# Kernel tuning notes

Measured on AMD Instinct MI355X. Metric: run time of the kernel, lower is better.

The kernel has to match this reference:

```python
import jax, jax.numpy as jnp
import numpy as np

N_NODES = 100000
N_EDGES = 1600000
N_FEAT = 128
HIDDEN = 128
EMB = 256
N_GROUPS = 16
N_GRAPHS = 512


def gcn_conv(x, edge_index, W, b, num_nodes):
    # PyG GCNConv: x' = D^{-1/2} (A + I) D^{-1/2} (x W) + b
    h = x @ W                                   # [N, out]
    loop = jnp.arange(num_nodes, dtype=edge_index.dtype)
    src = jnp.concatenate([edge_index[0], loop])
    dst = jnp.concatenate([edge_index[1], loop])
    ones = jnp.ones(src.shape[0], dtype=h.dtype)
    deg = jax.ops.segment_sum(ones, dst, num_segments=num_nodes)  # >=1 due to self loops
    dinv = jax.lax.rsqrt(deg)
    norm = dinv[src] * dinv[dst]                # [E+N]
    msg = h[src] * norm[:, None]                # gather + scale
    out = jax.ops.segment_sum(msg, dst, num_segments=num_nodes)   # scatter-add
    return out + b


def global_mean_pool(x, batch, num_graphs):
    s = jax.ops.segment_sum(x, batch, num_segments=num_graphs)
    cnt = jax.ops.segment_sum(jnp.ones(x.shape[0], dtype=x.dtype), batch, num_segments=num_graphs)
    return s / jnp.maximum(cnt, 1.0)[:, None]


def setup_inputs() -> dict:
    key = jax.random.key(0)
    ks = jax.random.split(key, 10)
    x = jax.random.normal(ks[0], (N_NODES, N_FEAT), dtype=jnp.float32)
    edge_index = jax.random.randint(ks[1], (2, N_EDGES), 0, N_NODES, dtype=jnp.int64 if jax.config.jax_enable_x64 else jnp.int32)
    batch = jnp.sort(jax.random.randint(ks[2], (N_NODES,), 0, N_GRAPHS))
    def glorot(k, shape):
        lim = np.sqrt(6.0 / (shape[0] + shape[1]))
        return jax.random.uniform(k, shape, jnp.float32, -lim, lim)
    W1 = glorot(ks[3], (N_FEAT, HIDDEN)); b1 = jnp.zeros((HIDDEN,), jnp.float32)
    W2 = glorot(ks[4], (HIDDEN, EMB));    b2 = jnp.zeros((EMB,), jnp.float32)
    Wg = glorot(ks[5], (EMB, N_GROUPS));  bg = jnp.zeros((N_GROUPS,), jnp.float32)
    return {"x": x, "edge_index": edge_index, "batch": batch, "num_graphs": N_GRAPHS,
            "W1": W1, "b1": b1, "W2": W2, "b2": b2, "Wg": Wg, "bg": bg}


def reference(x, edge_index, batch, num_graphs, W1, b1, W2, b2, Wg, bg):
    n = x.shape[0]
    h = jax.nn.relu(gcn_conv(x, edge_index, W1, b1, n))
    # dropout(p=0.5) is identity in eval mode
    h = gcn_conv(h, edge_index, W2, b2, n)
    emb = global_mean_pool(h, batch, num_graphs)      # [G, EMB]
    group_logits = emb @ Wg + bg                      # [G, N_GROUPS]
    return (emb, group_logits)
```

## Files before the change

### kernel.cpp

```cpp
#include <hip/hip_runtime.h>
#include <hip/hip_fp16.h>


#define TPB 256
#define CHUNK 4096
#define MAXB 512
#define SUBS 8

typedef _Float16 half8 __attribute__((ext_vector_type(8)));
typedef float floatx4 __attribute__((ext_vector_type(4)));

__device__ __forceinline__ void exscan512(int* a, int* part, int t) {
    int x0 = a[2 * t], x1 = a[2 * t + 1];
    part[t] = x0 + x1;
    __syncthreads();
    for (int off = 1; off < 256; off <<= 1) {
        int v = (t >= off) ? part[t - off] : 0;
        __syncthreads();
        part[t] += v;
        __syncthreads();
    }
    int base = (t > 0) ? part[t - 1] : 0;
    a[2 * t] = base;
    a[2 * t + 1] = base + x0;
    __syncthreads();
}

__global__ __launch_bounds__(256) void k1_bucket(const int* __restrict__ ei, int E,
                                                 int B, int nchunks,
                                                 uint2* __restrict__ sorted,
                                                 int* __restrict__ histT,
                                                 int* __restrict__ sstartT,
                                                 int* __restrict__ bucketTot) {
    __shared__ int hcnt[MAXB], hoff[MAXB], hcur[MAXB], part[256];
    int c = blockIdx.x, t = threadIdx.x;
    int e0 = c * CHUNK;
    int m = E - e0; if (m > CHUNK) m = CHUNK;
    for (int i = t; i < MAXB; i += 256) { hcnt[i] = 0; hcur[i] = 0; }
    __syncthreads();
    for (int i = t; i < m; i += 256)
        atomicAdd(&hcnt[ei[E + e0 + i] >> 8], 1);
    __syncthreads();
    for (int i = t; i < MAXB; i += 256) hoff[i] = hcnt[i];
    __syncthreads();
    exscan512(hoff, part, t);
    for (int i = t; i < B; i += 256) {
        histT[(size_t)i * nchunks + c]   = hcnt[i];
        sstartT[(size_t)i * nchunks + c] = e0 + hoff[i];
        if (hcnt[i] > 0) atomicAdd(&bucketTot[i], hcnt[i]);
    }
    __syncthreads();
    for (int i = t; i < m; i += 256) {
        int src = ei[e0 + i], dst = ei[E + e0 + i];
        int b = dst >> 8;
        int pos = e0 + hoff[b] + atomicAdd(&hcur[b], 1);
        sorted[pos] = make_uint2((unsigned)src, (unsigned)dst);
    }
}

__global__ void k2_scanB(const int* __restrict__ bucketTot, int B,
                         int* __restrict__ bucketBase) {
    __shared__ int a[MAXB], part[256];
    int t = threadIdx.x;
    a[t]       = (t < B) ? bucketTot[t] : 0;
    a[t + 256] = (t + 256 < B) ? bucketTot[t + 256] : 0;
    __syncthreads();
    exscan512(a, part, t);
    if (t < B) bucketBase[t] = a[t];
    if (t + 256 < B) bucketBase[t + 256] = a[t + 256];
    if (t == 255) bucketBase[B] = part[255];
}

#define SLICE_SETUP                                                             \
    int b = blockIdx.x, sub = blockIdx.y, t = threadIdx.x;                      \
    int cpg = (nchunks + SUBS - 1) / SUBS;                                      \
    int c0 = sub * cpg;                                                         \
    int c1 = c0 + cpg; if (c1 > nchunks) c1 = nchunks;                          \
    int nc = c1 - c0; if (nc < 0) nc = 0;                                       \
    if (t < nc) {                                                               \
        slen[t]   = histT[(size_t)b * nchunks + c0 + t];                        \
        sstart[t] = sstartT[(size_t)b * nchunks + c0 + t];                      \
    }                                                                           \
    __syncthreads();                                                            \
    if (t == 0) {                                                               \
        int run = 0;                                                            \
        for (int i2 = 0; i2 < nc; ++i2) { soff[i2] = run; run += slen[i2]; }    \
        soff[nc] = run;                                                         \
    }                                                                           \
    __syncthreads();                                                            \
    int T = soff[nc];

#define SLICE_EDGE(i)                                                           \
    int lo = 0, hi = nc - 1;                                                    \
    while (lo < hi) { int mid = (lo + hi + 1) >> 1;                             \
                      if (soff[mid] <= (i)) lo = mid; else hi = mid - 1; }      \
    uint2 e = sorted[sstart[lo] + ((i) - soff[lo])];

__global__ __launch_bounds__(256) void k3a_deg(const uint2* __restrict__ sorted,
                                               const int* __restrict__ histT,
                                               const int* __restrict__ sstartT,
                                               int* __restrict__ deg,
                                               int n, int nchunks) {
    __shared__ int slen[64], sstart[64], soff[65];
    __shared__ int ncnt[256];
    SLICE_SETUP
    ncnt[t] = 0;
    __syncthreads();
    int vb = b << 8;
    for (int i = t; i < T; i += 256) {
        SLICE_EDGE(i)
        atomicAdd(&ncnt[(int)e.y - vb], 1);
    }
    __syncthreads();
    int v = vb + t;
    if (v < n && ncnt[t] > 0) atomicAdd(&deg[v], ncnt[t]);
}

__global__ __launch_bounds__(256) void k3b_offs(const int* __restrict__ deg,
                                                const int* __restrict__ bucketBase,
                                                const int* __restrict__ batch,
                                                int* __restrict__ offs,
                                                float* __restrict__ dinv,
                                                int* __restrict__ cnt, int n) {
    __shared__ int a[512], part[256];
    int b = blockIdx.x, t = threadIdx.x;
    int v = (b << 8) + t;
    int dg = (v < n) ? deg[v] : 0;
    a[t] = dg; a[t + 256] = 0;
    __syncthreads();
    exscan512(a, part, t);
    if (v < n) {
        offs[v] = bucketBase[b] + a[t];
        dinv[v] = rsqrtf((float)(dg + 1));
        atomicAdd(&cnt[batch[v]], 1);
    }
}

__global__ __launch_bounds__(256) void k3c_scatter(const uint2* __restrict__ sorted,
                                                   const int* __restrict__ histT,
                                                   const int* __restrict__ sstartT,
                                                   const int* __restrict__ offs,
                                                   int* __restrict__ cursor,
                                                   int* __restrict__ adj, int nchunks) {
    __shared__ int slen[64], sstart[64], soff[65];
    SLICE_SETUP
    for (int i = t; i < T; i += 256) {
        SLICE_EDGE(i)
        int dst = (int)e.y;
        int pos = offs[dst] + atomicAdd(&cursor[dst], 1);
        adj[pos] = (int)e.x;
    }
}

__global__ void prep_wt(const float* __restrict__ W, __half* __restrict__ Wt) {
    int t = blockIdx.x * blockDim.x + threadIdx.x;
    int c = t & 127, k = t >> 7;
    Wt[c * 128 + k] = __float2half(W[(size_t)k * 128 + c]);
}

__global__ __launch_bounds__(256) void gemm1_mfma(const float* __restrict__ X,
                                                  const __half* __restrict__ Wt,
                                                  const float* __restrict__ dinv,
                                                  __half* __restrict__ out, int n) {
    __shared__ __align__(16) unsigned char As[64 * 128 * 2];
    __shared__ __align__(16) unsigned char Bs[128 * 128 * 2];
    int t = threadIdx.x;
    int wid = t >> 6, lane = t & 63;
    int qw = lane >> 4, lr = lane & 15;
    int rowBase = blockIdx.x * 64;

#pragma unroll
    for (int c = 0; c < 4; ++c) {
        int id = c * 256 + t;
        int r = id >> 4, kc = id & 15;
        int gr = rowBase + r;
        float4 x0, x1;
        if (gr < n) {
            const float4* src = (const float4*)(X + (size_t)gr * 128 + kc * 8);
            x0 = src[0]; x1 = src[1];
        } else {
            x0 = make_float4(0.f, 0.f, 0.f, 0.f); x1 = x0;
        }
        __half2 h0 = __floats2half2_rn(x0.x, x0.y);
        __half2 h1 = __floats2half2_rn(x0.z, x0.w);
        __half2 h2 = __floats2half2_rn(x1.x, x1.y);
        __half2 h3 = __floats2half2_rn(x1.z, x1.w);
        uint4 w;
        w.x = *(unsigned int*)&h0; w.y = *(unsigned int*)&h1;
        w.z = *(unsigned int*)&h2; w.w = *(unsigned int*)&h3;
        int byte = (r * 256 + kc * 16) ^ ((r & 7) << 4);
        *(uint4*)(As + byte) = w;
    }
#pragma unroll
    for (int c = 0; c < 8; ++c) {
        int id = c * 256 + t;
        int cr = id >> 4, kc = id & 15;
        uint4 w = *(const uint4*)(Wt + (size_t)cr * 128 + kc * 8);
        int byte = (cr * 256 + kc * 16) ^ ((cr & 7) << 4);
        *(uint4*)(Bs + byte) = w;
    }
    __syncthreads();

    floatx4 acc[4][2] = {};
#pragma unroll
    for (int ks = 0; ks < 4; ++ks) {
        int kb = ks * 32 + qw * 8;
        half8 a[4], b[2];
#pragma unroll
        for (int m = 0; m < 4; ++m) {
            int row = m * 16 + lr;
            int byte = (row * 256 + kb * 2) ^ ((row & 7) << 4);
            a[m] = *(const half8*)(As + byte);
        }
#pragma unroll
        for (int nn = 0; nn < 2; ++nn) {
            int col = wid * 32 + nn * 16 + lr;
            int byte = (col * 256 + kb * 2) ^ ((col & 7) << 4);
            b[nn] = *(const half8*)(Bs + byte);
        }
#pragma unroll
        for (int m = 0; m < 4; ++m)
#pragma unroll
            for (int nn = 0; nn < 2; ++nn)
                acc[m][nn] = __builtin_amdgcn_mfma_f32_16x16x32_f16(a[m], b[nn], acc[m][nn], 0, 0, 0);
    }

#pragma unroll
    for (int m = 0; m < 4; ++m) {
#pragma unroll
        for (int q = 0; q < 4; ++q) {
            int gr = rowBase + m * 16 + qw * 4 + q;
            if (gr < n) {
                float dv = dinv[gr];
#pragma unroll
                for (int nn = 0; nn < 2; ++nn) {
                    int col = wid * 32 + nn * 16 + lr;
                    out[(size_t)gr * 128 + col] = __float2half(acc[m][nn][q] * dv);
                }
            }
        }
    }
}

__device__ __forceinline__ void acc_h2(unsigned int rv, float2& a) {
    float2 f = __half22float2(*(__half2*)&rv);
    a.x += f.x; a.y += f.y;
}
#define ROWP(buf, u) ((const unsigned int*)((buf) + (size_t)(u) * 128))

#define PIPE_GATHER(buf)                                                        \
    int nb = d >> 3;                                                            \
    int i = nb << 3;                                                            \
    if (nb > 0) {                                                               \
        int u0 = adj[start+0], u1 = adj[start+1], u2 = adj[start+2],            \
            u3 = adj[start+3], u4 = adj[start+4], u5 = adj[start+5],            \
            u6 = adj[start+6], u7 = adj[start+7];                               \
        unsigned c0 = ROWP(buf,u0)[lane], c1 = ROWP(buf,u1)[lane];              \
        unsigned c2 = ROWP(buf,u2)[lane], c3 = ROWP(buf,u3)[lane];              \
        unsigned c4 = ROWP(buf,u4)[lane], c5 = ROWP(buf,u5)[lane];              \
        unsigned c6 = ROWP(buf,u6)[lane], c7 = ROWP(buf,u7)[lane];              \
        for (int bq = 1; bq < nb; ++bq) {                                       \
            int bs = start + (bq << 3);                                         \
            int t0 = adj[bs+0], t1 = adj[bs+1], t2 = adj[bs+2], t3 = adj[bs+3]; \
            int t4 = adj[bs+4], t5 = adj[bs+5], t6 = adj[bs+6], t7 = adj[bs+7]; \
            unsigned n0 = ROWP(buf,t0)[lane], n1 = ROWP(buf,t1)[lane];          \
            unsigned n2 = ROWP(buf,t2)[lane], n3 = ROWP(buf,t3)[lane];          \
            unsigned n4 = ROWP(buf,t4)[lane], n5 = ROWP(buf,t5)[lane];          \
            unsigned n6 = ROWP(buf,t6)[lane], n7 = ROWP(buf,t7)[lane];          \
            acc_h2(c0, a0); acc_h2(c1, a1); acc_h2(c2, a2); acc_h2(c3, a3);     \
            acc_h2(c4, a0); acc_h2(c5, a1); acc_h2(c6, a2); acc_h2(c7, a3);     \
            c0 = n0; c1 = n1; c2 = n2; c3 = n3;                                 \
            c4 = n4; c5 = n5; c6 = n6; c7 = n7;                                 \
        }                                                                       \
        acc_h2(c0, a0); acc_h2(c1, a1); acc_h2(c2, a2); acc_h2(c3, a3);         \
        acc_h2(c4, a0); acc_h2(c5, a1); acc_h2(c6, a2); acc_h2(c7, a3);         \
    }                                                                           \
    for (; i + 3 < d; i += 4) {                                                 \
        int u0 = adj[start+i+0], u1 = adj[start+i+1];                           \
        int u2 = adj[start+i+2], u3 = adj[start+i+3];                           \
        unsigned r0 = ROWP(buf,u0)[lane], r1 = ROWP(buf,u1)[lane];              \
        unsigned r2 = ROWP(buf,u2)[lane], r3 = ROWP(buf,u3)[lane];              \
        acc_h2(r0, a0); acc_h2(r1, a1); acc_h2(r2, a2); acc_h2(r3, a3);         \
    }                                                                           \
    for (; i < d; ++i) acc_h2(ROWP(buf, adj[start + i])[lane], a0);

__global__ void gather1(const __half* __restrict__ hs, const int* __restrict__ adj,
                        const int* __restrict__ offs, const int* __restrict__ deg,
                        const float* __restrict__ dinv, const float* __restrict__ b1,
                        __half* __restrict__ gs, int n) {
    int wave = threadIdx.x >> 6;
    int lane = threadIdx.x & 63;
    int v = blockIdx.x * 4 + wave;
    if (v >= n) return;
    float2 a0 = make_float2(0.f, 0.f), a1 = a0, a2 = a0, a3 = a0;
    acc_h2(ROWP(hs, v)[lane], a0);
    int start = __builtin_amdgcn_readfirstlane(offs[v]);
    int d     = __builtin_amdgcn_readfirstlane(deg[v]);
    PIPE_GATHER(hs)
    float accx = (a0.x + a1.x) + (a2.x + a3.x);
    float accy = (a0.y + a1.y) + (a2.y + a3.y);
    float dv = dinv[v];
    float2 bb = ((const float2*)b1)[lane];
    float g0 = fmaxf(accx * dv + bb.x, 0.f) * dv;
    float g1 = fmaxf(accy * dv + bb.y, 0.f) * dv;
    __half2 h = __floats2half2_rn(g0, g1);
    ((unsigned int*)(gs + (size_t)v * 128))[lane] = *(unsigned int*)&h;
}

__global__ void gather2_pool(const __half* __restrict__ gs, const int* __restrict__ adj,
                             const int* __restrict__ offs, const int* __restrict__ deg,
                             const float* __restrict__ dinv, const int* __restrict__ batch,
                             float* __restrict__ poolsum, int n) {
    __shared__ float poolacc[128];
    int t = threadIdx.x;
    int wave = t >> 6;
    int lane = t & 63;
    if (t < 128) poolacc[t] = 0.f;
    int gref = batch[blockIdx.x * 4];
    __syncthreads();
    int v = blockIdx.x * 4 + wave;
    if (v < n) {
        float2 a0 = make_float2(0.f, 0.f), a1 = a0, a2 = a0, a3 = a0;
        acc_h2(ROWP(gs, v)[lane], a0);
        int start = __builtin_amdgcn_readfirstlane(offs[v]);
        int d     = __builtin_amdgcn_readfirstlane(deg[v]);
        PIPE_GATHER(gs)
        float accx = (a0.x + a1.x) + (a2.x + a3.x);
        float accy = (a0.y + a1.y) + (a2.y + a3.y);
        float dv = dinv[v];
        int g = batch[v];
        if (g == gref) {
            atomicAdd(&poolacc[lane * 2 + 0], accx * dv);
            atomicAdd(&poolacc[lane * 2 + 1], accy * dv);
        } else {
            float* p = poolsum + (size_t)g * 128;
            atomicAdd(&p[lane * 2 + 0], accx * dv);
            atomicAdd(&p[lane * 2 + 1], accy * dv);
        }
    }
    __syncthreads();
    if (t < 128) {
        float s = poolacc[t];
        if (s != 0.f) atomicAdd(&poolsum[(size_t)gref * 128 + t], s);
    }
}

__global__ void head(const float* __restrict__ poolsum, const int* __restrict__ cnt,
                     const float* __restrict__ W2, const float* __restrict__ b2,
                     const float* __restrict__ Wg, const float* __restrict__ bg,
                     float* __restrict__ out, int G) {
    __shared__ float pm[128];
    __shared__ float emb[256];
    int g = blockIdx.x, t = threadIdx.x;
    float inv = 1.f / fmaxf((float)cnt[g], 1.f);
    if (t < 128) pm[t] = poolsum[(size_t)g * 128 + t] * inv;
    __syncthreads();
    float acc = b2[t];
    for (int k = 0; k < 128; ++k) acc += pm[k] * W2[k * 256 + t];
    out[(size_t)g * 256 + t] = acc;
    emb[t] = acc;
    __syncthreads();
    if (t < 16) {
        float a = bg[t];
        for (int j = 0; j < 256; ++j) a += emb[j] * Wg[j * 16 + t];
        out[(size_t)G * 256 + g * 16 + t] = a;
    }
}

extern "C" void kernel_launch(void* const* d_in, const int* in_sizes, int n_in,
                              void* d_out, int out_size, void* d_ws, size_t ws_size,
                              hipStream_t stream) {
    const float* x     = (const float*)d_in[0];
    const int*   ei    = (const int*)d_in[1];
    const int*   batch = (const int*)d_in[2];
    const float* W1    = (const float*)d_in[4];
    const float* b1    = (const float*)d_in[5];
    const float* W2    = (const float*)d_in[6];
    const float* b2    = (const float*)d_in[7];
    const float* Wg    = (const float*)d_in[8];
    const float* bg    = (const float*)d_in[9];
    float* out = (float*)d_out;

    int n = in_sizes[0] / 128;
    int E = in_sizes[1] / 2;
    int G = out_size / (256 + 16);
    int B = (n + 255) >> 8;
    int nchunks = (E + CHUNK - 1) / CHUNK;

    char* ws = (char*)d_ws;
    auto alloc = [&](size_t bytes) {
        char* p = ws;
        ws += (bytes + 255) & ~(size_t)255;
        return p;
    };
    int*    deg       = (int*)alloc((size_t)n * 4);
    float*  dinv      = (float*)alloc((size_t)n * 4);
    int*    offs      = (int*)alloc((size_t)n * 4);
    int*    cursor    = (int*)alloc((size_t)n * 4);
    int*    adj       = (int*)alloc((size_t)E * 4);
    uint2*  sorted    = (uint2*)alloc((size_t)E * 8);
    int*    histT     = (int*)alloc((size_t)B * nchunks * 4);
    int*    sstartT   = (int*)alloc((size_t)B * nchunks * 4);
    int*    bucketTot = (int*)alloc((size_t)(B + 1) * 4);
    int*    bucketBase= (int*)alloc((size_t)(B + 1) * 4);
    int*    cnt       = (int*)alloc((size_t)G * 4);
    float*  poolsum   = (float*)alloc((size_t)G * 128 * 4);
    __half* Wt        = (__half*)alloc(128 * 128 * 2);
    __half* hs1       = (__half*)alloc((size_t)n * 128 * 2);
    __half* gs1       = (__half*)alloc((size_t)n * 128 * 2);

    hipMemsetAsync(deg, 0, (size_t)n * 4, stream);
    hipMemsetAsync(cursor, 0, (size_t)n * 4, stream);
    hipMemsetAsync(bucketTot, 0, (size_t)(B + 1) * 4, stream);
    hipMemsetAsync(cnt, 0, (size_t)G * 4, stream);
    hipMemsetAsync(poolsum, 0, (size_t)G * 128 * 4, stream);

    k1_bucket<<<nchunks, 256, 0, stream>>>(ei, E, B, nchunks, sorted, histT, sstartT, bucketTot);
    k2_scanB<<<1, 256, 0, stream>>>(bucketTot, B, bucketBase);
    k3a_deg<<<dim3(B, SUBS), 256, 0, stream>>>(sorted, histT, sstartT, deg, n, nchunks);
    k3b_offs<<<B, 256, 0, stream>>>(deg, bucketBase, batch, offs, dinv, cnt, n);
    k3c_scatter<<<dim3(B, SUBS), 256, 0, stream>>>(sorted, histT, sstartT, offs, cursor, adj, nchunks);

    prep_wt<<<64, TPB, 0, stream>>>(W1, Wt);
    gemm1_mfma<<<(n + 63) / 64, 256, 0, stream>>>(x, Wt, dinv, hs1, n);
    gather1<<<(n + 3) / 4, 256, 0, stream>>>(hs1, adj, offs, deg, dinv, b1, gs1, n);
    gather2_pool<<<(n + 3) / 4, 256, 0, stream>>>(gs1, adj, offs, deg, dinv, batch, poolsum, n);
    head<<<G, 256, 0, stream>>>(poolsum, cnt, W2, b2, Wg, bg, out, G);
}
```

Measured before the change: 367.7 us.

## Fold degree count into bucketing, pack sorted edges, drop scan kernels

Degree counting moves into k1_bucket as global atomics, which removes the separate k3a_deg pass over the sorted edges. The bucket-base scan kernel is dropped and each k3b block instead reduces the bucket totals before its own bucket. Sorted edges are packed into 32 bits (17-bit src plus 8-bit local dst), which halves that traffic. The histT/sstartT layout becomes chunk-major and the five memsets are merged into one. Risks: 1.6M global atomics on deg, and the packing assumes fewer than 131072 nodes.

```diff
diff --git a/kernel.cpp b/kernel.cpp
--- a/kernel.cpp
+++ b/kernel.cpp
@@ -6,6 +6,7 @@
 #define CHUNK 4096
 #define MAXB 512
 #define SUBS 8
+#define SRCMASK 0x1FFFF
 
 typedef _Float16 half8 __attribute__((ext_vector_type(8)));
 typedef float floatx4 __attribute__((ext_vector_type(4)));
@@ -28,25 +29,29 @@
 
 __global__ __launch_bounds__(256) void k1_bucket(const int* __restrict__ ei, int E,
                                                  int B, int nchunks,
-                                                 uint2* __restrict__ sorted,
+                                                 unsigned* __restrict__ sorted,
                                                  int* __restrict__ histT,
                                                  int* __restrict__ sstartT,
-                                                 int* __restrict__ bucketTot) {
+                                                 int* __restrict__ bucketTot,
+                                                 int* __restrict__ deg) {
     __shared__ int hcnt[MAXB], hoff[MAXB], hcur[MAXB], part[256];
     int c = blockIdx.x, t = threadIdx.x;
     int e0 = c * CHUNK;
     int m = E - e0; if (m > CHUNK) m = CHUNK;
     for (int i = t; i < MAXB; i += 256) { hcnt[i] = 0; hcur[i] = 0; }
     __syncthreads();
-    for (int i = t; i < m; i += 256)
-        atomicAdd(&hcnt[ei[E + e0 + i] >> 8], 1);
+    for (int i = t; i < m; i += 256) {
+        int dst = ei[E + e0 + i];
+        atomicAdd(&hcnt[dst >> 8], 1);
+        atomicAdd(&deg[dst], 1);
+    }
     __syncthreads();
     for (int i = t; i < MAXB; i += 256) hoff[i] = hcnt[i];
     __syncthreads();
     exscan512(hoff, part, t);
     for (int i = t; i < B; i += 256) {
-        histT[(size_t)i * nchunks + c]   = hcnt[i];
-        sstartT[(size_t)i * nchunks + c] = e0 + hoff[i];
+        histT[(size_t)c * B + i]   = hcnt[i];
+        sstartT[(size_t)c * B + i] = e0 + hoff[i];
         if (hcnt[i] > 0) atomicAdd(&bucketTot[i], hcnt[i]);
     }
     __syncthreads();
@@ -54,101 +59,78 @@
         int src = ei[e0 + i], dst = ei[E + e0 + i];
         int b = dst >> 8;
         int pos = e0 + hoff[b] + atomicAdd(&hcur[b], 1);
-        sorted[pos] = make_uint2((unsigned)src, (unsigned)dst);
-    }
-}
-
-__global__ void k2_scanB(const int* __restrict__ bucketTot, int B,
-                         int* __restrict__ bucketBase) {
-    __shared__ int a[MAXB], part[256];
-    int t = threadIdx.x;
-    a[t]       = (t < B) ? bucketTot[t] : 0;
-    a[t + 256] = (t + 256 < B) ? bucketTot[t + 256] : 0;
-    __syncthreads();
-    exscan512(a, part, t);
-    if (t < B) bucketBase[t] = a[t];
-    if (t + 256 < B) bucketBase[t + 256] = a[t + 256];
-    if (t == 255) bucketBase[B] = part[255];
-}
-
-#define SLICE_SETUP                                                             \
-    int b = blockIdx.x, sub = blockIdx.y, t = threadIdx.x;                      \
-    int cpg = (nchunks + SUBS - 1) / SUBS;                                      \
-    int c0 = sub * cpg;                                                         \
-    int c1 = c0 + cpg; if (c1 > nchunks) c1 = nchunks;                          \
-    int nc = c1 - c0; if (nc < 0) nc = 0;                                       \
-    if (t < nc) {                                                               \
-        slen[t]   = histT[(size_t)b * nchunks + c0 + t];                        \
-        sstart[t] = sstartT[(size_t)b * nchunks + c0 + t];                      \
-    }                                                                           \
-    __syncthreads();                                                            \
-    if (t == 0) {                                                               \
-        int run = 0;                                                            \
-        for (int i2 = 0; i2 < nc; ++i2) { soff[i2] = run; run += slen[i2]; }    \
-        soff[nc] = run;                                                         \
-    }                                                                           \
-    __syncthreads();                                                            \
-    int T = soff[nc];
-
-#define SLICE_EDGE(i)                                                           \
-    int lo = 0, hi = nc - 1;                                                    \
-    while (lo < hi) { int mid = (lo + hi + 1) >> 1;                             \
-                      if (soff[mid] <= (i)) lo = mid; else hi = mid - 1; }      \
-    uint2 e = sorted[sstart[lo] + ((i) - soff[lo])];
-
-__global__ __launch_bounds__(256) void k3a_deg(const uint2* __restrict__ sorted,
-                                               const int* __restrict__ histT,
-                                               const int* __restrict__ sstartT,
-                                               int* __restrict__ deg,
-                                               int n, int nchunks) {
-    __shared__ int slen[64], sstart[64], soff[65];
-    __shared__ int ncnt[256];
-    SLICE_SETUP
-    ncnt[t] = 0;
-    __syncthreads();
-    int vb = b << 8;
-    for (int i = t; i < T; i += 256) {
-        SLICE_EDGE(i)
-        atomicAdd(&ncnt[(int)e.y - vb], 1);
-    }
-    __syncthreads();
-    int v = vb + t;
-    if (v < n && ncnt[t] > 0) atomicAdd(&deg[v], ncnt[t]);
+        sorted[pos] = (unsigned)src | ((unsigned)(dst & 255) << 17);
+    }
 }
 
 __global__ __launch_bounds__(256) void k3b_offs(const int* __restrict__ deg,
-                                                const int* __restrict__ bucketBase,
+                                                const int* __restrict__ bucketTot,
                                                 const int* __restrict__ batch,
                                                 int* __restrict__ offs,
                                                 float* __restrict__ dinv,
                                                 int* __restrict__ cnt, int n) {
     __shared__ int a[512], part[256];
+    __shared__ int baseS;
     int b = blockIdx.x, t = threadIdx.x;
+    int s = 0;
+    for (int i = t; i < b; i += 256) s += bucketTot[i];
+    part[t] = s;
+    __syncthreads();
+    for (int off = 128; off > 0; off >>= 1) {
+        if (t < off) part[t] += part[t + off];
+        __syncthreads();
+    }
+    if (t == 0) baseS = part[0];
+    __syncthreads();
+    int base = baseS;
     int v = (b << 8) + t;
     int dg = (v < n) ? deg[v] : 0;
     a[t] = dg; a[t + 256] = 0;
     __syncthreads();
     exscan512(a, part, t);
     if (v < n) {
-        offs[v] = bucketBase[b] + a[t];
+        offs[v] = base + a[t];
         dinv[v] = rsqrtf((float)(dg + 1));
         atomicAdd(&cnt[batch[v]], 1);
     }
 }
 
-__global__ __launch_bounds__(256) void k3c_scatter(const uint2* __restrict__ sorted,
+__global__ __launch_bounds__(256) void k3c_scatter(const unsigned* __restrict__ sorted,
                                                    const int* __restrict__ histT,
                                                    const int* __restrict__ sstartT,
                                                    const int* __restrict__ offs,
                                                    int* __restrict__ cursor,
-                                                   int* __restrict__ adj, int nchunks) {
+                                                   int* __restrict__ adj,
+                                                   int B, int nchunks) {
     __shared__ int slen[64], sstart[64], soff[65];
-    SLICE_SETUP
+    int b = blockIdx.x, sub = blockIdx.y, t = threadIdx.x;
+    int cpg = (nchunks + SUBS - 1) / SUBS;
+    int c0 = sub * cpg;
+    int c1 = c0 + cpg; if (c1 > nchunks) c1 = nchunks;
+    int nc = c1 - c0; if (nc < 0) nc = 0;
+    if (t < nc) {
+        slen[t]   = histT[(size_t)(c0 + t) * B + b];
+        sstart[t] = sstartT[(size_t)(c0 + t) * B + b];
+    }
+    __syncthreads();
+    if (t == 0) {
+        int run = 0;
+        for (int i2 = 0; i2 < nc; ++i2) { soff[i2] = run; run += slen[i2]; }
+        soff[nc] = run;
+    }
+    __syncthreads();
+    int T = soff[nc];
+    int vb = b << 8;
     for (int i = t; i < T; i += 256) {
-        SLICE_EDGE(i)
-        int dst = (int)e.y;
+        int lo = 0, hi = nc - 1;
+        while (lo < hi) {
+            int mid = (lo + hi + 1) >> 1;
+            if (soff[mid] <= i) lo = mid; else hi = mid - 1;
+        }
+        unsigned w = sorted[sstart[lo] + (i - soff[lo])];
+        int dst = vb + (int)((w >> 17) & 255);
         int pos = offs[dst] + atomicAdd(&cursor[dst], 1);
-        adj[pos] = (int)e.x;
+        adj[pos] = (int)(w & SRCMASK);
     }
 }
 
@@ -393,33 +375,30 @@
         ws += (bytes + 255) & ~(size_t)255;
         return p;
     };
+    char*   zbase     = ws;
     int*    deg       = (int*)alloc((size_t)n * 4);
-    float*  dinv      = (float*)alloc((size_t)n * 4);
-    int*    offs      = (int*)alloc((size_t)n * 4);
     int*    cursor    = (int*)alloc((size_t)n * 4);
-    int*    adj       = (int*)alloc((size_t)E * 4);
-    uint2*  sorted    = (uint2*)alloc((size_t)E * 8);
-    int*    histT     = (int*)alloc((size_t)B * nchunks * 4);
-    int*    sstartT   = (int*)alloc((size_t)B * nchunks * 4);
     int*    bucketTot = (int*)alloc((size_t)(B + 1) * 4);
-    int*    bucketBase= (int*)alloc((size_t)(B + 1) * 4);
     int*    cnt       = (int*)alloc((size_t)G * 4);
     float*  poolsum   = (float*)alloc((size_t)G * 128 * 4);
-    __half* Wt        = (__half*)alloc(128 * 128 * 2);
-    __half* hs1       = (__half*)alloc((size_t)n * 128 * 2);
-    __half* gs1       = (__half*)alloc((size_t)n * 128 * 2);
-
-    hipMemsetAsync(deg, 0, (size_t)n * 4, stream);
-    hipMemsetAsync(cursor, 0, (size_t)n * 4, stream);
-    hipMemsetAsync(bucketTot, 0, (size_t)(B + 1) * 4, stream);
-    hipMemsetAsync(cnt, 0, (size_t)G * 4, stream);
-    hipMemsetAsync(poolsum, 0, (size_t)G * 128 * 4, stream);
-
-    k1_bucket<<<nchunks, 256, 0, stream>>>(ei, E, B, nchunks, sorted, histT, sstartT, bucketTot);
-    k2_scanB<<<1, 256, 0, stream>>>(bucketTot, B, bucketBase);
-    k3a_deg<<<dim3(B, SUBS), 256, 0, stream>>>(sorted, histT, sstartT, deg, n, nchunks);
-    k3b_offs<<<B, 256, 0, stream>>>(deg, bucketBase, batch, offs, dinv, cnt, n);
-    k3c_scatter<<<dim3(B, SUBS), 256, 0, stream>>>(sorted, histT, sstartT, offs, cursor, adj, nchunks);
+    size_t  zbytes    = (size_t)(ws - zbase);
+    float*    dinv    = (float*)alloc((size_t)n * 4);
+    int*      offs    = (int*)alloc((size_t)n * 4);
+    int*      adj     = (int*)alloc((size_t)E * 4);
+    unsigned* sorted  = (unsigned*)alloc((size_t)E * 4);
+    int*      histT   = (int*)alloc((size_t)B * nchunks * 4);
+    int*      sstartT = (int*)alloc((size_t)B * nchunks * 4);
+    __half*   Wt      = (__half*)alloc(128 * 128 * 2);
+    __half*   hs1     = (__half*)alloc((size_t)n * 128 * 2);
+    __half*   gs1     = (__half*)alloc((size_t)n * 128 * 2);
+
+    hipMemsetAsync(zbase, 0, zbytes, stream);
+
+    k1_bucket<<<nchunks, 256, 0, stream>>>(ei, E, B, nchunks, sorted, histT, sstartT,
+                                           bucketTot, deg);
+    k3b_offs<<<B, 256, 0, stream>>>(deg, bucketTot, batch, offs, dinv, cnt, n);
+    k3c_scatter<<<dim3(B, SUBS), 256, 0, stream>>>(sorted, histT, sstartT, offs, cursor,
+                                                   adj, B, nchunks);
 
     prep_wt<<<64, TPB, 0, stream>>>(W1, Wt);
     gemm1_mfma<<<(n + 63) / 64, 256, 0, stream>>>(x, Wt, dinv, hs1, n);
```

Result: slower. 408.3 us (+11.0%).
